# Kernel optimization log

Measured on AMD Instinct MI355X. Metric: run time of the kernel, lower is better.

## Reference

```python
import jax, jax.numpy as jnp
import numpy as np

B, C, H, W = 8, 256, 64, 64
DQK = 16  # int(sqrt(out_channels))


def setup_inputs() -> dict:
    key = jax.random.key(0)
    ks = jax.random.split(key, 8)
    s_in = 1.0 / np.sqrt(C)
    return {
        "x": jax.random.normal(ks[0], (B, C, H, W), dtype=jnp.float32),
        "Wf": jax.random.normal(ks[1], (DQK, C), dtype=jnp.float32) * s_in,
        "bf": jnp.zeros((DQK,), dtype=jnp.float32),
        "Wg": jax.random.normal(ks[2], (DQK, C), dtype=jnp.float32) * s_in,
        "bg": jnp.zeros((DQK,), dtype=jnp.float32),
        "Wh": jax.random.normal(ks[3], (C, C), dtype=jnp.float32) * s_in,
        "bh": jnp.zeros((C,), dtype=jnp.float32),
        # original inits attention_multiplier to 0.0; use small nonzero so output depends on attention path
        "gamma": jnp.float32(0.5),
    }


def reference(x, Wf, bf, Wg, bg, Wh, bh, gamma):
    b, c, h, w = x.shape
    hw = h * w
    # 1x1 convs == per-pixel channel projections
    f = (jnp.einsum('bchw,oc->bohw', x, Wf) + bf[None, :, None, None]).reshape(b, -1, hw)  # [B,DQK,HW]
    g = (jnp.einsum('bchw,oc->bohw', x, Wg) + bg[None, :, None, None]).reshape(b, -1, hw)  # [B,DQK,HW]
    hh = (jnp.einsum('bchw,oc->bohw', x, Wh) + bh[None, :, None, None]).reshape(b, -1, hw)  # [B,C,HW]
    # s[b,n,m] = sum_k g[b,k,n] * f[b,k,m]  -> [B,HW,HW]
    s = jnp.einsum('bkn,bkm->bnm', g, f)
    beta = jax.nn.softmax(s, axis=-1)
    # o = beta @ h^T, then transpose back to channel-first: [B,C,HW]
    o = jnp.einsum('bnm,bcm->bcn', beta, hh)
    return gamma * o.reshape(x.shape) + x
```

## Files before the change

### kernel.cpp

```cpp
#include <hip/hip_runtime.h>
#include <math.h>

#define BATCH 8
#define CH    256
#define HWN   4096
#define DQK   16

typedef __attribute__((ext_vector_type(8))) short short8;
typedef __attribute__((ext_vector_type(4))) float float4v;

#define L2E 1.4426950408889634f

__device__ __forceinline__ unsigned short f2bf(float f) {
    union { float f; unsigned int u; } v; v.f = f;
    unsigned int r = v.u + 0x7FFF + ((v.u >> 16) & 1);
    return (unsigned short)(r >> 16);
}
__device__ __forceinline__ unsigned int cvtpk(float lo, float hi) {
    unsigned int r;
    asm("v_cvt_pk_bf16_f32 %0, %1, %2" : "=v"(r) : "v"(lo), "v"(hi));
    return r;
}
__device__ __forceinline__ float ex2(float x) {
#if __has_builtin(__builtin_amdgcn_exp2f)
    return __builtin_amdgcn_exp2f(x);
#else
    return exp2f(x);
#endif
}
__device__ __forceinline__ void lds_barrier() {
    asm volatile("s_waitcnt lgkmcnt(0)" ::: "memory");
    __builtin_amdgcn_s_barrier();
}
__device__ __forceinline__ int perm_ft(int m) {
    return (m & ~28) | ((m & 24) >> 1) | ((m & 4) << 2);
}

__global__ __launch_bounds__(256) void wcast_kernel(
    const float* __restrict__ Wf, const float* __restrict__ bf_,
    const float* __restrict__ Wg, const float* __restrict__ bg,
    const float* __restrict__ Wh, const float* __restrict__ bh,
    unsigned short* __restrict__ Wbf, float* __restrict__ bcat)
{
    const int r = blockIdx.x;
    const int t = threadIdx.x;
    const float* src = (r < 16) ? (Wf + r*CH) : (r < 32) ? (Wg + (r-16)*CH) : (Wh + (r-32)*CH);
    Wbf[r*CH + t] = f2bf(src[t]);
    if (t == 0) bcat[r] = (r < 16) ? bf_[r] : (r < 32) ? bg[r-16] : bh[r-32];
}

__global__ __launch_bounds__(256) void xt_kernel(const float* __restrict__ x,
                                                 unsigned short* __restrict__ xt)
{
    const int t  = threadIdx.x;
    const int p0 = blockIdx.x * 64;
    const int c0 = blockIdx.y * 64;
    const int b  = blockIdx.z;
    __shared__ unsigned short tile[64][74];
    const int col4 = (t & 15) * 4;
    const int cr   = t >> 4;
    #pragma unroll
    for (int j = 0; j < 4; j++) {
        int c = cr + j*16;
        float4 v = *(const float4*)&x[(size_t)(b*CH + c0 + c)*HWN + p0 + col4];
        unsigned int u01 = cvtpk(v.x, v.y), u23 = cvtpk(v.z, v.w);
        tile[col4+0][c] = (unsigned short)u01;
        tile[col4+1][c] = (unsigned short)(u01 >> 16);
        tile[col4+2][c] = (unsigned short)u23;
        tile[col4+3][c] = (unsigned short)(u23 >> 16);
    }
    __syncthreads();
    const int pr = t >> 2;
    const int cb = (t & 3) * 16;
    unsigned int outv[8];
    #pragma unroll
    for (int i = 0; i < 8; i++)
        outv[i] = *(const unsigned int*)&tile[pr][cb + 2*i];
    unsigned short* dst = &xt[(size_t)(b*HWN + p0 + pr)*CH + c0 + cb];
    *(uint4*)dst       = *(uint4*)&outv[0];
    *(uint4*)(dst + 8) = *(uint4*)&outv[4];
}

__global__ __launch_bounds__(256, 6) void proj_kernel(
    const unsigned short* __restrict__ xt, const unsigned short* __restrict__ Wbf,
    const float* __restrict__ bcat,
    unsigned short* __restrict__ ft, unsigned short* __restrict__ g,
    unsigned short* __restrict__ h3)
{
    const int t      = threadIdx.x;
    const int px0    = blockIdx.x * 64;
    const int b      = blockIdx.y;
    const int rtbase = blockIdx.z * 6;
    const int lane = t & 63, w = t >> 6, l15 = lane & 15, quad = lane >> 4;

    float4v acc[6];
    #pragma unroll
    for (int rt = 0; rt < 6; rt++) acc[rt] = (float4v){0.f,0.f,0.f,0.f};

    const unsigned short* xrow = &xt[((size_t)(b*HWN + px0 + w*16 + l15))*CH + quad*8];
    const unsigned short* wrow = &Wbf[(size_t)l15*CH + quad*8];

    #pragma unroll
    for (int ks = 0; ks < 8; ks++) {
        short8 afrag = *(const short8*)&xrow[ks*32];
        #pragma unroll
        for (int rt = 0; rt < 6; rt++) {
            short8 bfrag = *(const short8*)&wrow[(size_t)(rtbase + rt)*16*CH + ks*32];
            acc[rt] = __builtin_amdgcn_mfma_f32_16x16x32_bf16(afrag, bfrag, acc[rt], 0, 0, 0);
        }
    }

    const int pxl = px0 + w*16 + quad*4;
    const int mt  = (px0 >> 5) + (w >> 1);
    const int sub = ((w & 1)*2 + (quad >> 1))*128 + l15*8 + (quad & 1)*4;
    #pragma unroll
    for (int rt = 0; rt < 6; rt++) {
        const int R = rtbase + rt;
        if (R == 0) {
            float bv = bcat[l15];
            const int s0 = perm_ft(pxl);
            unsigned int p01 = cvtpk((acc[rt][0] + bv)*L2E, (acc[rt][1] + bv)*L2E);
            unsigned int p23 = cvtpk((acc[rt][2] + bv)*L2E, (acc[rt][3] + bv)*L2E);
            unsigned short* fp0 = &ft[((size_t)b*HWN + s0)*32];
            fp0[l15]       = (unsigned short)p01;         fp0[16 + l15]  = 0;
            fp0[32 + l15]  = (unsigned short)(p01 >> 16); fp0[48 + l15]  = 0;
            fp0[64 + l15]  = (unsigned short)p23;         fp0[80 + l15]  = 0;
            fp0[96 + l15]  = (unsigned short)(p23 >> 16); fp0[112 + l15] = 0;
        } else if (R == 1) {
            float bv = bcat[16 + l15];
            unsigned int a01 = cvtpk(acc[rt][0] + bv, acc[rt][1] + bv);
            unsigned int a23 = cvtpk(acc[rt][2] + bv, acc[rt][3] + bv);
            *(uint2*)&g[(size_t)(b*DQK + l15)*HWN + pxl] = make_uint2(a01, a23);
        } else {
            float bv = bcat[R*16 + l15];
            unsigned int u0 = cvtpk(acc[rt][0] + bv, acc[rt][1] + bv);
            unsigned int u1 = cvtpk(acc[rt][2] + bv, acc[rt][3] + bv);
            *(uint2*)&h3[(((size_t)((b*128 + mt)*16 + (R-2))) << 9) + sub] = make_uint2(u0, u1);
        }
    }
}

__global__ __launch_bounds__(512, 4) void attn_kernel(
    const unsigned short* __restrict__ ft, const unsigned short* __restrict__ g,
    const unsigned short* __restrict__ h3, const float* __restrict__ x,
    const float* __restrict__ gamma_p, float* __restrict__ out)
{
    const int t    = threadIdx.x;
    const int b    = blockIdx.x & 7;
    const int q0   = (blockIdx.x >> 3) * 64;
    const int lane = t & 63, w = t >> 6, l15 = lane & 15, quad = lane >> 4;
    const int qt_w = w >> 1, half = w & 1;

    __shared__ __align__(16) uint4 pB[2][2][4][64];
    __shared__ float l_l[4][16][2];

    union { short8 v; unsigned short u[8]; } gfrag;
    #pragma unroll
    for (int j = 0; j < 8; j++) {
        int k = quad*8 + j;
        gfrag.u[j] = (k < DQK) ? g[(size_t)(b*DQK + k)*HWN + q0 + qt_w*16 + l15] : (unsigned short)0;
    }

    const unsigned short* ftb = ft + (size_t)b*HWN*32;
    const unsigned short* h3b = h3 + ((size_t)b << 20);

    short8 fr[2][2], hr[2][2][2];
    float4v acc[2][4];
    #pragma unroll
    for (int i = 0; i < 2; i++)
        #pragma unroll
        for (int j = 0; j < 4; j++) acc[i][j] = (float4v){0.f,0.f,0.f,0.f};
    float l_acc = 0.f;
    uint4 P;

    #pragma unroll
    for (int j = 0; j < 2; j++)
        fr[0][j] = *(const short8*)&ftb[(size_t)((half*2 + j)*16 + l15)*32 + quad*8];
    {
        float4v z = {0.f,0.f,0.f,0.f};
        float4v s0v = __builtin_amdgcn_mfma_f32_16x16x32_bf16(fr[0][0], gfrag.v, z, 0, 0, 0);
        float4v s1v = __builtin_amdgcn_mfma_f32_16x16x32_bf16(fr[0][1], gfrag.v, z, 0, 0, 0);
        float e0 = ex2(s0v[0]), e1 = ex2(s0v[1]), e2 = ex2(s0v[2]), e3 = ex2(s0v[3]);
        float e4 = ex2(s1v[0]), e5 = ex2(s1v[1]), e6 = ex2(s1v[2]), e7 = ex2(s1v[3]);
        l_acc += (e0 + e1) + (e2 + e3) + (e4 + e5) + (e6 + e7);
        P = make_uint4(cvtpk(e0, e1), cvtpk(e2, e3), cvtpk(e4, e5), cvtpk(e6, e7));
    }
    #pragma unroll
    for (int j = 0; j < 2; j++)
        fr[1][j] = *(const short8*)&ftb[(size_t)(64 + (half*2 + j)*16 + l15)*32 + quad*8];
    #pragma unroll
    for (int grp = 0; grp < 2; grp++)
        #pragma unroll
        for (int ctl = 0; ctl < 2; ctl++)
            hr[0][grp][ctl] = *(const short8*)&h3b[(((size_t)(grp*16 + w*2 + ctl)) << 9) + lane*8];

#define ATTN_STEP(u, i, DO_NEXT) do {                                          \
    if (DO_NEXT) {                                                             \
      const int nh = (i) + 1;                                                  \
      _Pragma("unroll")                                                        \
      for (int grp = 0; grp < 2; grp++)                                        \
        _Pragma("unroll")                                                      \
        for (int ctl = 0; ctl < 2; ctl++)                                      \
          hr[(u)^1][grp][ctl] = *(const short8*)&h3b[(((size_t)((nh*2 + grp)*16 + w*2 + ctl)) << 9) + lane*8]; \
    }                                                                          \
    pB[u][half][qt_w][lane] = P;                                               \
    lds_barrier();                                                             \
    if (DO_NEXT) {                                                             \
      const int nf = (i) + 2;                                                  \
      _Pragma("unroll")                                                        \
      for (int j = 0; j < 2; j++)                                              \
        fr[u][j] = *(const short8*)&ftb[(size_t)(nf*64 + (half*2 + j)*16 + l15)*32 + quad*8]; \
      float4v z = {0.f,0.f,0.f,0.f};                                           \
      float4v s0v = __builtin_amdgcn_mfma_f32_16x16x32_bf16(fr[(u)^1][0], gfrag.v, z, 0, 0, 0); \
      float4v s1v = __builtin_amdgcn_mfma_f32_16x16x32_bf16(fr[(u)^1][1], gfrag.v, z, 0, 0, 0); \
      float e0 = ex2(s0v[0]), e1 = ex2(s0v[1]), e2 = ex2(s0v[2]), e3 = ex2(s0v[3]); \
      float e4 = ex2(s1v[0]), e5 = ex2(s1v[1]), e6 = ex2(s1v[2]), e7 = ex2(s1v[3]); \
      l_acc += (e0 + e1) + (e2 + e3) + (e4 + e5) + (e6 + e7);                  \
      P = make_uint4(cvtpk(e0, e1), cvtpk(e2, e3), cvtpk(e4, e5), cvtpk(e6, e7)); \
    }                                                                          \
    __builtin_amdgcn_s_setprio(1);                                             \
    _Pragma("unroll")                                                          \
    for (int grp = 0; grp < 2; grp++) {                                        \
      _Pragma("unroll")                                                        \
      for (int qt = 0; qt < 4; qt++) {                                         \
        union { uint4 uu; short8 v; } bq;                                      \
        bq.uu = pB[u][grp][qt][lane];                                          \
        _Pragma("unroll")                                                      \
        for (int ctl = 0; ctl < 2; ctl++)                                      \
          acc[ctl][qt] = __builtin_amdgcn_mfma_f32_16x16x32_bf16(hr[u][grp][ctl], bq.v, acc[ctl][qt], 0, 0, 0); \
      }                                                                        \
    }                                                                          \
    __builtin_amdgcn_s_setprio(0);                                             \
  } while (0)

    for (int i0 = 0; i0 < 62; i0 += 2) {
        ATTN_STEP(0, i0, 1);
        ATTN_STEP(1, i0 + 1, 1);
    }
    ATTN_STEP(0, 62, 1);
    ATTN_STEP(1, 63, 0);
#undef ATTN_STEP

    l_acc += __shfl_xor(l_acc, 16, 64);
    l_acc += __shfl_xor(l_acc, 32, 64);
    if (quad == 0) l_l[qt_w][l15][half] = l_acc;
    __syncthreads();

    const float gamma = *gamma_p;
    float linv[4];
    #pragma unroll
    for (int qt = 0; qt < 4; qt++) linv[qt] = 1.f / (l_l[qt][l15][0] + l_l[qt][l15][1]);
    #pragma unroll
    for (int ctl = 0; ctl < 2; ctl++) {
        #pragma unroll
        for (int r = 0; r < 4; r++) {
            int c = w*32 + ctl*16 + quad*4 + r;
            size_t base = (size_t)(b*CH + c)*HWN + q0;
            #pragma unroll
            for (int qt = 0; qt < 4; qt++) {
                size_t o = base + qt*16 + l15;
                out[o] = gamma * acc[ctl][qt][r] * linv[qt] + x[o];
            }
        }
    }
}

extern "C" void kernel_launch(void* const* d_in, const int* in_sizes, int n_in,
                              void* d_out, int out_size, void* d_ws, size_t ws_size,
                              hipStream_t stream) {
    const float* x     = (const float*)d_in[0];
    const float* Wf    = (const float*)d_in[1];
    const float* bf_   = (const float*)d_in[2];
    const float* Wg    = (const float*)d_in[3];
    const float* bg    = (const float*)d_in[4];
    const float* Wh    = (const float*)d_in[5];
    const float* bh    = (const float*)d_in[6];
    const float* gamma = (const float*)d_in[7];
    float* out = (float*)d_out;

    unsigned short* xt   = (unsigned short*)d_ws;
    unsigned short* ftp  = xt  + (size_t)BATCH*HWN*CH;
    unsigned short* g    = ftp + (size_t)BATCH*HWN*32;
    unsigned short* h3   = g   + (size_t)BATCH*DQK*HWN;
    unsigned short* Wbf  = h3  + (size_t)BATCH*128*16*512;
    float*          bcat = (float*)(Wbf + 288*CH);

    wcast_kernel<<<dim3(288), 256, 0, stream>>>(Wf, bf_, Wg, bg, Wh, bh, Wbf, bcat);
    xt_kernel<<<dim3(HWN/64, CH/64, BATCH), 256, 0, stream>>>(x, xt);
    proj_kernel<<<dim3(HWN/64, BATCH, 3), 256, 0, stream>>>(xt, Wbf, bcat, ftp, g, h3);
    attn_kernel<<<dim3((HWN/64)*BATCH), 512, 0, stream>>>(ftp, g, h3, x, gamma, out);
}
```

Measured before the change: 215.3 us.

## Quad-buffer P tiles in LDS so softmax writes overlap PV MFMAs

Grows the shared P buffer from two to four stages. Each step now writes the next tile's P right after computing it, before the MFMA accumulation of the previous tile, instead of writing it just before the barrier. Global loads for both h and f are grouped ahead of the barrier behind a sched_barrier, and the four B-fragment LDS reads are hoisted ahead of the MFMA chain. The intent is to remove the store-then-barrier dependency that serialized exp computation with PV MFMAs, at the cost of more LDS per block, which may affect occupancy.

```diff
diff --git a/kernel.cpp b/kernel.cpp
--- a/kernel.cpp
+++ b/kernel.cpp
@@ -151,7 +151,7 @@
     const int lane = t & 63, w = t >> 6, l15 = lane & 15, quad = lane >> 4;
     const int qt_w = w >> 1, half = w & 1;
 
-    __shared__ __align__(16) uint4 pB[2][2][4][64];
+    __shared__ __align__(16) uint4 pB[4][2][4][64];
     __shared__ float l_l[4][16][2];
 
     union { short8 v; unsigned short u[8]; } gfrag;
@@ -185,6 +185,7 @@
         l_acc += (e0 + e1) + (e2 + e3) + (e4 + e5) + (e6 + e7);
         P = make_uint4(cvtpk(e0, e1), cvtpk(e2, e3), cvtpk(e4, e5), cvtpk(e6, e7));
     }
+    pB[0][half][qt_w][lane] = P;
     #pragma unroll
     for (int j = 0; j < 2; j++)
         fr[1][j] = *(const short8*)&ftb[(size_t)(64 + (half*2 + j)*16 + l15)*32 + quad*8];
@@ -194,7 +195,7 @@
         for (int ctl = 0; ctl < 2; ctl++)
             hr[0][grp][ctl] = *(const short8*)&h3b[(((size_t)(grp*16 + w*2 + ctl)) << 9) + lane*8];
 
-#define ATTN_STEP(u, i, DO_NEXT) do {                                          \
+#define ATTN_STEP(u, up, un, i, DO_NEXT) do {                                  \
     if (DO_NEXT) {                                                             \
       const int nh = (i) + 1;                                                  \
       _Pragma("unroll")                                                        \
@@ -202,14 +203,14 @@
         _Pragma("unroll")                                                      \
         for (int ctl = 0; ctl < 2; ctl++)                                      \
           hr[(u)^1][grp][ctl] = *(const short8*)&h3b[(((size_t)((nh*2 + grp)*16 + w*2 + ctl)) << 9) + lane*8]; \
-    }                                                                          \
-    pB[u][half][qt_w][lane] = P;                                               \
-    lds_barrier();                                                             \
-    if (DO_NEXT) {                                                             \
       const int nf = (i) + 2;                                                  \
       _Pragma("unroll")                                                        \
       for (int j = 0; j < 2; j++)                                              \
         fr[u][j] = *(const short8*)&ftb[(size_t)(nf*64 + (half*2 + j)*16 + l15)*32 + quad*8]; \
+      __builtin_amdgcn_sched_barrier(0);                                       \
+    }                                                                          \
+    lds_barrier();                                                             \
+    if (DO_NEXT) {                                                             \
       float4v z = {0.f,0.f,0.f,0.f};                                           \
       float4v s0v = __builtin_amdgcn_mfma_f32_16x16x32_bf16(fr[(u)^1][0], gfrag.v, z, 0, 0, 0); \
       float4v s1v = __builtin_amdgcn_mfma_f32_16x16x32_bf16(fr[(u)^1][1], gfrag.v, z, 0, 0, 0); \
@@ -217,28 +218,37 @@
       float e4 = ex2(s1v[0]), e5 = ex2(s1v[1]), e6 = ex2(s1v[2]), e7 = ex2(s1v[3]); \
       l_acc += (e0 + e1) + (e2 + e3) + (e4 + e5) + (e6 + e7);                  \
       P = make_uint4(cvtpk(e0, e1), cvtpk(e2, e3), cvtpk(e4, e5), cvtpk(e6, e7)); \
+      pB[un][half][qt_w][lane] = P;                                            \
     }                                                                          \
     __builtin_amdgcn_s_setprio(1);                                             \
     _Pragma("unroll")                                                          \
     for (int grp = 0; grp < 2; grp++) {                                        \
+      union { uint4 uu; short8 v; } bq0, bq1, bq2, bq3;                        \
+      bq0.uu = pB[up][grp][0][lane];                                           \
+      bq1.uu = pB[up][grp][1][lane];                                           \
+      bq2.uu = pB[up][grp][2][lane];                                           \
+      bq3.uu = pB[up][grp][3][lane];                                           \
       _Pragma("unroll")                                                        \
-      for (int qt = 0; qt < 4; qt++) {                                         \
-        union { uint4 uu; short8 v; } bq;                                      \
-        bq.uu = pB[u][grp][qt][lane];                                          \
-        _Pragma("unroll")                                                      \
-        for (int ctl = 0; ctl < 2; ctl++)                                      \
-          acc[ctl][qt] = __builtin_amdgcn_mfma_f32_16x16x32_bf16(hr[u][grp][ctl], bq.v, acc[ctl][qt], 0, 0, 0); \
+      for (int ctl = 0; ctl < 2; ctl++) {                                      \
+        acc[ctl][0] = __builtin_amdgcn_mfma_f32_16x16x32_bf16(hr[u][grp][ctl], bq0.v, acc[ctl][0], 0, 0, 0); \
+        acc[ctl][1] = __builtin_amdgcn_mfma_f32_16x16x32_bf16(hr[u][grp][ctl], bq1.v, acc[ctl][1], 0, 0, 0); \
+        acc[ctl][2] = __builtin_amdgcn_mfma_f32_16x16x32_bf16(hr[u][grp][ctl], bq2.v, acc[ctl][2], 0, 0, 0); \
+        acc[ctl][3] = __builtin_amdgcn_mfma_f32_16x16x32_bf16(hr[u][grp][ctl], bq3.v, acc[ctl][3], 0, 0, 0); \
       }                                                                        \
     }                                                                          \
     __builtin_amdgcn_s_setprio(0);                                             \
   } while (0)
 
-    for (int i0 = 0; i0 < 62; i0 += 2) {
-        ATTN_STEP(0, i0, 1);
-        ATTN_STEP(1, i0 + 1, 1);
-    }
-    ATTN_STEP(0, 62, 1);
-    ATTN_STEP(1, 63, 0);
+    for (int i0 = 0; i0 < 60; i0 += 4) {
+        ATTN_STEP(0, 0, 1, i0 + 0, 1);
+        ATTN_STEP(1, 1, 2, i0 + 1, 1);
+        ATTN_STEP(0, 2, 3, i0 + 2, 1);
+        ATTN_STEP(1, 3, 0, i0 + 3, 1);
+    }
+    ATTN_STEP(0, 0, 1, 60, 1);
+    ATTN_STEP(1, 1, 2, 61, 1);
+    ATTN_STEP(0, 2, 3, 62, 1);
+    ATTN_STEP(1, 3, 0, 63, 0);
 #undef ATTN_STEP
 
     l_acc += __shfl_xor(l_acc, 16, 64);
```

Result: slower. 254.7 us (+18.3%).
